# Kernel optimization log

Hardware: AMD Instinct MI355X
Metric: run time of the kernel (lower is better)

Reference implementation:

```python
import jax, jax.numpy as jnp
import numpy as np

B, L = 64, 16384
INTERP_FACTOR = 0.25
WINDOW, STEP = 256, 64
ALPHA, BETA, TEMP = 0.12, 0.9, 1.0
A = -0.75  # PyTorch grid_sample bicubic coefficient


def _cubic_w(t):
    # cubic convolution kernel (Keys, a=-0.75), matches torch bicubic
    at = jnp.abs(t)
    w_near = ((A + 2.0) * at - (A + 3.0)) * at * at + 1.0          # |t| <= 1
    w_far = ((A * at - 5.0 * A) * at + 8.0 * A) * at - 4.0 * A      # 1 < |t| < 2
    return jnp.where(at <= 1.0, w_near, jnp.where(at < 2.0, w_far, 0.0))


def cubic_interpolate_1d(signal, interp_factor):
    # equivalent to the grid_sample(mode='bicubic', padding='border',
    # align_corners=True) hack on a (B,1,1,n) image: y-direction is identity.
    b, n = signal.shape
    num_points = int((n - 1) / interp_factor) + 1
    x = jnp.linspace(0.0, 1.0, num_points) * (n - 1)                 # sample coords
    i0 = jnp.floor(x).astype(jnp.int32)
    frac = x - i0.astype(x.dtype)
    offs = jnp.arange(-1, 3)                                         # 4 taps
    idx = jnp.clip(i0[:, None] + offs[None, :], 0, n - 1)            # (P,4) border pad
    w = _cubic_w(frac[:, None] - offs[None, :].astype(x.dtype))      # (P,4)
    taps = signal[:, idx]                                            # (B,P,4)
    return jnp.einsum('bpk,pk->bp', taps, w)


def _apply_kernels(x):
    # gamma-normalized mix: 0.5*polynomial(deg=2,off=1.3) + 0.5*gaussian(c=0.7,s=1.0)
    poly = (x + 1.3) ** 2
    gauss = jnp.exp(-0.5 * ((x - 0.7) / 1.0) ** 2)
    return 0.5 * poly + 0.5 * gauss


def soft_minimum(a, b, temperature):
    b = jnp.broadcast_to(b, a.shape)
    stacked = jnp.stack([-a * temperature, -b * temperature], axis=0)
    return -jax.nn.logsumexp(stacked, axis=0) / temperature


def _forward(signal):
    interp = cubic_interpolate_1d(signal, INTERP_FACTOR)             # (B, n)
    n = interp.shape[1]
    n_windows = (n - WINDOW) // STEP + 1
    starts = jnp.arange(n_windows) * STEP
    idx = starts[:, None] + jnp.arange(WINDOW)[None, :]              # (nw, W)
    windows = interp[:, idx]                                         # (B, nw, W)
    kw = _apply_kernels(windows)                                     # per-window kernel eval
    M = jnp.abs(jnp.fft.fft(kw, axis=-1))                            # magnitude spectrum
    Mmax = jnp.max(M, axis=-1, keepdims=True)
    thr = ALPHA * Mmax                                               # local threshold
    mask = jax.nn.sigmoid((M - thr) * TEMP)                          # soft threshold
    Mt = M * mask
    return soft_minimum(Mt, BETA * Mmax, TEMP)                       # smart min (B, nw, W)


def setup_inputs() -> dict:
    key = jax.random.key(0)
    return {"signal": jax.random.normal(key, (B, L), dtype=jnp.float32)}


def reference(signal):
    return _forward(signal)
```

## Files before the change

### kernel.cpp

```cpp
#include <hip/hip_runtime.h>
#include <math.h>

#define LSIG 16384
#define NWIN 1020
#define WTILE 64
#define MTILES 16
#define STRIP 1088
#define PMAXOFF (STRIP * 8)
#define LDSBYTES (PMAXOFF + WTILE * 4 * 4)

typedef __attribute__((ext_vector_type(8))) short short8;
typedef __attribute__((ext_vector_type(4))) float f32x4;
typedef __attribute__((ext_vector_type(4))) unsigned short us4;

__device__ __forceinline__ unsigned short f2b(float f) {
    union { float f; unsigned int u; } x; x.f = f;
    unsigned int r = x.u + 0x7fffu + ((x.u >> 16) & 1u);
    return (unsigned short)(r >> 16);
}

__device__ __forceinline__ float kwf(float x) {
    float p = x + 1.3f;
    float d = x - 0.7f;
    return fmaf(0.5f * p, p, 0.5f * __expf(-0.5f * d * d));
}

__device__ __forceinline__ float smin_fast(float Mv, float thr, float bb) {
    float t = __expf(thr - Mv);
    float Mt = Mv * __builtin_amdgcn_rcpf(1.0f + t);
    return fminf(Mt, bb);
}

__global__ void build_dft(unsigned short* __restrict__ Bf) {
    const int t = blockIdx.x;
    const int c = threadIdx.x;
    const int bin = ((c >> 6) << 5) + (((c >> 5) & 1) << 4) + (c & 15);
    const int kind = (c >> 4) & 1;
    float v;
    if (c == 16) {
        v = (t & 1) ? -1.0f : 1.0f;
    } else {
        const int prod = (bin * t) & 255;
        const float a = (float)prod * 0.024543692606170f;
        v = (kind == 0) ? __cosf(a) : -__sinf(a);
    }
    Bf[(((t >> 3) * 256) + c) * 8 + (t & 7)] = f2b(v);
}

__global__ __launch_bounds__(256, 4) void ntfa_gemm(const float* __restrict__ sig,
                                                    const unsigned short* __restrict__ Bf,
                                                    float* __restrict__ out) {
    __shared__ __align__(16) char lds[LDSBYTES];
    float* pmax_s = (float*)(lds + PMAXOFF);

    const int tid = threadIdx.x;
    const int lane = tid & 63;
    const int wid = tid >> 6;
    const int wn0 = wid * 64;
    const int lm = lane & 15;
    const int lg = lane >> 4;
    const bool spec = (wid == 0) && (lm == 0);

    const int mtile = blockIdx.x;
    const int b = blockIdx.y;
    const int S0q = mtile * 1024;
    const float* srow = sig + (size_t)b * LSIG;

#pragma unroll
    for (int k = 0; k < 5; ++k) {
        int q = tid + k * 256;
        if (q < STRIP) {
            int gq = S0q + q;
            float o0 = 0.f, o1 = 0.f, o2 = 0.f, o3 = 0.f;
            if (gq <= 16383) {
                float ta = srow[gq - 1 < 0 ? 0 : gq - 1];
                float tb = srow[gq];
                float tc = srow[gq + 1 > 16383 ? 16383 : gq + 1];
                float td = srow[gq + 2 > 16383 ? 16383 : gq + 2];
                float x0 = tb;
                float x1 = fmaf(ta, -0.10546875f, fmaf(tb, 0.87890625f,
                            fmaf(tc, 0.26171875f, td * -0.03515625f)));
                float x2 = fmaf(ta, -0.09375f, fmaf(tb, 0.59375f,
                            fmaf(tc, 0.59375f, td * -0.09375f)));
                float x3 = fmaf(ta, -0.03515625f, fmaf(tb, 0.26171875f,
                            fmaf(tc, 0.87890625f, td * -0.10546875f)));
                o0 = kwf(x0); o1 = kwf(x1); o2 = kwf(x2); o3 = kwf(x3);
                if (gq == 16383) { o1 = 0.f; o2 = 0.f; o3 = 0.f; }
            }
            us4 pk; pk.x = f2b(o0); pk.y = f2b(o1); pk.z = f2b(o2); pk.w = f2b(o3);
            int la = q * 8;
            la ^= ((la >> 7) & 7) << 4;
            *(us4*)(lds + la) = pk;
        }
    }
    __syncthreads();

    f32x4 acc[4][4] = {};
    short8 bcur[4], bnxt[4];
#pragma unroll
    for (int nt = 0; nt < 4; ++nt)
        bcur[nt] = *(const short8*)(Bf + ((0 * 4 + lg) * 256 + wn0 + nt * 16 + lm) * 8);
#pragma unroll
    for (int ks = 0; ks < 8; ++ks) {
        if (ks < 7) {
#pragma unroll
            for (int nt = 0; nt < 4; ++nt)
                bnxt[nt] = *(const short8*)(Bf + (((ks + 1) * 4 + lg) * 256 + wn0 + nt * 16 + lm) * 8);
        }
        short8 afr[4];
#pragma unroll
        for (int mt = 0; mt < 4; ++mt) {
            int sb = ((mt * 16 + lm) * 64 + ks * 32 + lg * 8) * 2;
            sb ^= ((sb >> 7) & 7) << 4;
            afr[mt] = *(const short8*)(lds + sb);
        }
#pragma unroll
        for (int mt = 0; mt < 4; ++mt)
#pragma unroll
            for (int nt = 0; nt < 4; ++nt)
                acc[mt][nt] = __builtin_amdgcn_mfma_f32_16x16x32_bf16(
                    afr[mt], bcur[nt], acc[mt][nt], 0, 0, 0);
        if (ks < 7) {
#pragma unroll
            for (int nt = 0; nt < 4; ++nt) bcur[nt] = bnxt[nt];
        }
    }

    float M[4][2][4], M128[4][4], pm[4][4];
#pragma unroll
    for (int mt = 0; mt < 4; ++mt) {
#pragma unroll
        for (int k = 0; k < 2; ++k)
#pragma unroll
            for (int r = 0; r < 4; ++r) {
                float re = acc[mt][2 * k][r];
                float im = acc[mt][2 * k + 1][r];
                if (k == 0 && spec) {
                    M[mt][0][r] = fabsf(re);
                    M128[mt][r] = fabsf(im);
                } else {
                    M[mt][k][r] = __builtin_amdgcn_sqrtf(fmaf(re, re, im * im));
                }
            }
#pragma unroll
        for (int r = 0; r < 4; ++r) {
            float p = fmaxf(M[mt][0][r], M[mt][1][r]);
            if (spec) p = fmaxf(p, M128[mt][r]);
            pm[mt][r] = p;
        }
    }
#pragma unroll
    for (int msk = 1; msk < 16; msk <<= 1)
#pragma unroll
        for (int mt = 0; mt < 4; ++mt)
#pragma unroll
            for (int r = 0; r < 4; ++r)
                pm[mt][r] = fmaxf(pm[mt][r], __shfl_xor(pm[mt][r], msk));

    if (lm == 0) {
#pragma unroll
        for (int mt = 0; mt < 4; ++mt)
#pragma unroll
            for (int r = 0; r < 4; ++r)
                pmax_s[(mt * 16 + lg * 4 + r) * 4 + wid] = pm[mt][r];
    }
    __syncthreads();

    const int w0 = mtile * WTILE;
#pragma unroll
    for (int mt = 0; mt < 4; ++mt) {
#pragma unroll
        for (int r = 0; r < 4; ++r) {
            const int win = mt * 16 + lg * 4 + r;
            const int gw = w0 + win;
            if (gw < NWIN) {
                const float* pp = pmax_s + win * 4;
                const float Mx = fmaxf(fmaxf(pp[0], pp[1]), fmaxf(pp[2], pp[3]));
                const float thr = 0.12f * Mx;
                const float bb = 0.9f * Mx;
                float* row = out + (((size_t)(b * NWIN + gw)) << 8);
#pragma unroll
                for (int k = 0; k < 2; ++k) {
                    const int bin = wid * 32 + k * 16 + lm;
                    const float outv = smin_fast(M[mt][k][r], thr, bb);
                    row[bin] = outv;
                    if (bin >= 1) row[256 - bin] = outv;
                    if (k == 0 && spec)
                        row[128] = smin_fast(M128[mt][r], thr, bb);
                }
            }
        }
    }
}

extern "C" void kernel_launch(void* const* d_in, const int* in_sizes, int n_in,
                              void* d_out, int out_size, void* d_ws, size_t ws_size,
                              hipStream_t stream) {
    const float* sig = (const float*)d_in[0];
    float* out = (float*)d_out;
    unsigned short* Bf = (unsigned short*)d_ws;

    hipLaunchKernelGGL(build_dft, dim3(256), dim3(256), 0, stream, Bf);
    hipLaunchKernelGGL(ntfa_gemm, dim3(MTILES, 64), dim3(256), 0, stream, sig, Bf, out);
}
```

Before: 32.12 us.

## Give each wave whole windows and stage output rows in LDS for coalesced stores

Work is now split across waves by window rather than by frequency bin. Each wave computes all 256 bins for 16 windows, so the per-window max is found with in-wave shuffles, and the block-wide LDS max exchange and its __syncthreads go away. Each wave builds the full symmetric output row in a padded LDS buffer and writes it out as 16-byte non-temporal vector stores instead of scattered scalar stores. In exchange, every wave loads the whole DFT matrix from global memory (4x more B traffic per block), the register prefetch of B is dropped, and 16 accumulators per lane raise register pressure.

Result: slower. 37.70 us (+17.4%).

```diff
diff --git a/kernel.cpp b/kernel.cpp
--- a/kernel.cpp
+++ b/kernel.cpp
@@ -6,8 +6,9 @@
 #define WTILE 64
 #define MTILES 16
 #define STRIP 1088
-#define PMAXOFF (STRIP * 8)
-#define LDSBYTES (PMAXOFF + WTILE * 4 * 4)
+#define RBSTRIDE 272
+#define RBOFF (STRIP * 8)
+#define LDSBYTES (RBOFF + 16 * RBSTRIDE * 4)
 
 typedef __attribute__((ext_vector_type(8))) short short8;
 typedef __attribute__((ext_vector_type(4))) float f32x4;
@@ -51,15 +52,12 @@
                                                     const unsigned short* __restrict__ Bf,
                                                     float* __restrict__ out) {
     __shared__ __align__(16) char lds[LDSBYTES];
-    float* pmax_s = (float*)(lds + PMAXOFF);
 
     const int tid = threadIdx.x;
     const int lane = tid & 63;
     const int wid = tid >> 6;
-    const int wn0 = wid * 64;
     const int lm = lane & 15;
     const int lg = lane >> 4;
-    const bool spec = (wid == 0) && (lm == 0);
 
     const int mtile = blockIdx.x;
     const int b = blockIdx.y;
@@ -95,99 +93,65 @@
     }
     __syncthreads();
 
-    f32x4 acc[4][4] = {};
-    short8 bcur[4], bnxt[4];
-#pragma unroll
-    for (int nt = 0; nt < 4; ++nt)
-        bcur[nt] = *(const short8*)(Bf + ((0 * 4 + lg) * 256 + wn0 + nt * 16 + lm) * 8);
+    const int wbase = mtile * WTILE + wid * 16;
+    f32x4 acc[16] = {};
 #pragma unroll
     for (int ks = 0; ks < 8; ++ks) {
-        if (ks < 7) {
+        int sb = ((wid * 16 + lm) * 64 + ks * 32 + lg * 8) * 2;
+        sb ^= ((sb >> 7) & 7) << 4;
+        const short8 afr = *(const short8*)(lds + sb);
 #pragma unroll
-            for (int nt = 0; nt < 4; ++nt)
-                bnxt[nt] = *(const short8*)(Bf + (((ks + 1) * 4 + lg) * 256 + wn0 + nt * 16 + lm) * 8);
-        }
-        short8 afr[4];
+        for (int h = 0; h < 2; ++h) {
+            short8 bf[8];
 #pragma unroll
-        for (int mt = 0; mt < 4; ++mt) {
-            int sb = ((mt * 16 + lm) * 64 + ks * 32 + lg * 8) * 2;
-            sb ^= ((sb >> 7) & 7) << 4;
-            afr[mt] = *(const short8*)(lds + sb);
-        }
+            for (int n8 = 0; n8 < 8; ++n8)
+                bf[n8] = *(const short8*)(Bf + ((ks * 4 + lg) * 256 + (h * 8 + n8) * 16 + lm) * 8);
 #pragma unroll
-        for (int mt = 0; mt < 4; ++mt)
-#pragma unroll
-            for (int nt = 0; nt < 4; ++nt)
-                acc[mt][nt] = __builtin_amdgcn_mfma_f32_16x16x32_bf16(
-                    afr[mt], bcur[nt], acc[mt][nt], 0, 0, 0);
-        if (ks < 7) {
-#pragma unroll
-            for (int nt = 0; nt < 4; ++nt) bcur[nt] = bnxt[nt];
+            for (int n8 = 0; n8 < 8; ++n8)
+                acc[h * 8 + n8] = __builtin_amdgcn_mfma_f32_16x16x32_bf16(
+                    afr, bf[n8], acc[h * 8 + n8], 0, 0, 0);
         }
     }
 
-    float M[4][2][4], M128[4][4], pm[4][4];
+    float* rw = (float*)(lds + RBOFF) + (wid * 4 + lg) * RBSTRIDE;
 #pragma unroll
-    for (int mt = 0; mt < 4; ++mt) {
+    for (int r = 0; r < 4; ++r) {
+        float mag[8], m128 = 0.f;
 #pragma unroll
-        for (int k = 0; k < 2; ++k)
+        for (int j = 0; j < 8; ++j) {
+            float re = acc[2 * j][r];
+            float im = acc[2 * j + 1][r];
+            if (j == 0 && lm == 0) {
+                mag[0] = fabsf(re);
+                m128 = fabsf(im);
+            } else {
+                mag[j] = __builtin_amdgcn_sqrtf(fmaf(re, re, im * im));
+            }
+        }
+        float mx = fmaxf(fmaxf(fmaxf(mag[0], mag[1]), fmaxf(mag[2], mag[3])),
+                         fmaxf(fmaxf(mag[4], mag[5]), fmaxf(mag[6], mag[7])));
+        if (lm == 0) mx = fmaxf(mx, m128);
 #pragma unroll
-            for (int r = 0; r < 4; ++r) {
-                float re = acc[mt][2 * k][r];
-                float im = acc[mt][2 * k + 1][r];
-                if (k == 0 && spec) {
-                    M[mt][0][r] = fabsf(re);
-                    M128[mt][r] = fabsf(im);
-                } else {
-                    M[mt][k][r] = __builtin_amdgcn_sqrtf(fmaf(re, re, im * im));
-                }
-            }
+        for (int msk = 1; msk < 16; msk <<= 1)
+            mx = fmaxf(mx, __shfl_xor(mx, msk));
+        const float thr = 0.12f * mx;
+        const float bb = 0.9f * mx;
 #pragma unroll
-        for (int r = 0; r < 4; ++r) {
-            float p = fmaxf(M[mt][0][r], M[mt][1][r]);
-            if (spec) p = fmaxf(p, M128[mt][r]);
-            pm[mt][r] = p;
+        for (int j = 0; j < 8; ++j) {
+            const float v = smin_fast(mag[j], thr, bb);
+            rw[16 * j + lm] = v;
+            rw[256 - 16 * j - lm] = v;
         }
-    }
+        if (lm == 0) rw[128] = smin_fast(m128, thr, bb);
+
+        const int gw = wbase + lg * 4 + r;
+        if (gw < NWIN) {
+            float* orow = out + (((size_t)(b * NWIN + gw)) << 8);
 #pragma unroll
-    for (int msk = 1; msk < 16; msk <<= 1)
-#pragma unroll
-        for (int mt = 0; mt < 4; ++mt)
-#pragma unroll
-            for (int r = 0; r < 4; ++r)
-                pm[mt][r] = fmaxf(pm[mt][r], __shfl_xor(pm[mt][r], msk));
-
-    if (lm == 0) {
-#pragma unroll
-        for (int mt = 0; mt < 4; ++mt)
-#pragma unroll
-            for (int r = 0; r < 4; ++r)
-                pmax_s[(mt * 16 + lg * 4 + r) * 4 + wid] = pm[mt][r];
-    }
-    __syncthreads();
-
-    const int w0 = mtile * WTILE;
-#pragma unroll
-    for (int mt = 0; mt < 4; ++mt) {
-#pragma unroll
-        for (int r = 0; r < 4; ++r) {
-            const int win = mt * 16 + lg * 4 + r;
-            const int gw = w0 + win;
-            if (gw < NWIN) {
-                const float* pp = pmax_s + win * 4;
-                const float Mx = fmaxf(fmaxf(pp[0], pp[1]), fmaxf(pp[2], pp[3]));
-                const float thr = 0.12f * Mx;
-                const float bb = 0.9f * Mx;
-                float* row = out + (((size_t)(b * NWIN + gw)) << 8);
-#pragma unroll
-                for (int k = 0; k < 2; ++k) {
-                    const int bin = wid * 32 + k * 16 + lm;
-                    const float outv = smin_fast(M[mt][k][r], thr, bb);
-                    row[bin] = outv;
-                    if (bin >= 1) row[256 - bin] = outv;
-                    if (k == 0 && spec)
-                        row[128] = smin_fast(M128[mt][r], thr, bb);
-                }
+            for (int i = 0; i < 4; ++i) {
+                const int c4 = i * 64 + lm * 4;
+                f32x4 v = *(const f32x4*)(rw + c4);
+                __builtin_nontemporal_store(v, (f32x4*)(orow + c4));
             }
         }
     }
```
